# Optimization experiments

Hardware: AMD Instinct MI355X
Metric: run time of the kernel (lower is better)

## Reference

```python
import jax, jax.numpy as jnp
import numpy as np

NUM_NODES = 1_000_000
HIDDEN = 256
NUM_GRAPHS = 1024


def setup_inputs() -> dict:
    key = jax.random.key(0)
    k_x, k_b, k_w1, k_b1, k_w2, k_b2 = jax.random.split(key, 6)
    x = jax.random.normal(k_x, (NUM_NODES, HIDDEN), dtype=jnp.float32)
    batch = jnp.sort(jax.random.randint(k_b, (NUM_NODES,), 0, NUM_GRAPHS, dtype=jnp.int64))
    h = HIDDEN // 2
    # torch Linear default init: U(-1/sqrt(fan_in), 1/sqrt(fan_in))
    s1 = 1.0 / np.sqrt(HIDDEN)
    s2 = 1.0 / np.sqrt(h)
    w1 = jax.random.uniform(k_w1, (HIDDEN, h), jnp.float32, -s1, s1)
    b1 = jax.random.uniform(k_b1, (h,), jnp.float32, -s1, s1)
    w2 = jax.random.uniform(k_w2, (h, 1), jnp.float32, -s2, s2)
    b2 = jax.random.uniform(k_b2, (1,), jnp.float32, -s2, s2)
    return {"x": x, "batch": batch, "w1": w1, "b1": b1, "w2": w2, "b2": b2}


def reference(x, batch, w1, b1, w2, b2):
    # attention MLP: Linear -> tanh -> Linear -> scalar score per node
    scores = (jnp.tanh(x @ w1 + b1) @ w2 + b2)[:, 0]  # [N]
    # segment softmax over nodes of each graph (numerically stable)
    seg_max = jax.ops.segment_max(scores, batch, num_segments=NUM_GRAPHS)  # [B]
    e = jnp.exp(scores - seg_max[batch])  # [N]
    denom = jax.ops.segment_sum(e, batch, num_segments=NUM_GRAPHS)  # [B]
    attn = e / denom[batch]  # [N]
    # attention-weighted scatter-add pooling -> [B, H]
    return jax.ops.segment_sum(x * attn[:, None], batch, num_segments=NUM_GRAPHS)
```

## Files before the change

kernel.cpp:

```cpp
#include <hip/hip_runtime.h>
#include <stdint.h>

#define N_NODES 1000000
#define HID 256
#define HH  128
#define NG  1024
#define TILE 32
#define CHUNK 1984
#define NBLOCKS ((N_NODES + CHUNK - 1) / CHUNK)

typedef short short8v __attribute__((ext_vector_type(8)));
typedef float f32x4 __attribute__((ext_vector_type(4)));

#define GLOBAL_AS __attribute__((address_space(1)))
#define LDS_AS    __attribute__((address_space(3)))

__device__ __forceinline__ unsigned short f2bf(float f){
  unsigned u = __float_as_uint(f);
  u += 0x7FFFu + ((u >> 16) & 1u);
  return (unsigned short)(u >> 16);
}

__device__ __forceinline__ float fast_tanh(float v){
  float e = __expf(2.f * v);
  return 1.f - 2.f / (e + 1.f);
}

__global__ void k_prep(const float* __restrict__ w1, unsigned short* __restrict__ w1f){
  int s = blockIdx.x * blockDim.x + threadIdx.x;
  if (s >= 4096) return;
  int nt = s >> 9, rem = s & 511, ks = rem >> 6, lane = rem & 63;
  int q = lane >> 4, c = lane & 15;
  union { unsigned short u[8]; uint4 v; } tmp;
  for (int i = 0; i < 8; ++i){
    int k = ks * 32 + q * 8 + i;
    int n = nt * 16 + c;
    tmp.u[i] = f2bf(w1[k * HH + n]);
  }
  *(uint4*)(w1f + (size_t)s * 8) = tmp.v;
}

__device__ __forceinline__ void stage_tile(const float* __restrict__ x, long node0,
                                           float* lds_tile, int wave, int lane){
  #pragma unroll
  for (int rr = 0; rr < 8; ++rr){
    int r = wave * 8 + rr;
    const float* gp = x + (size_t)(node0 + r) * HID + ((lane ^ (r & 15)) << 2);
    __builtin_amdgcn_global_load_lds(
        (const GLOBAL_AS unsigned int*)gp,
        (LDS_AS unsigned int*)(lds_tile + r * HID),
        16, 0, 0);
  }
}

__global__ __launch_bounds__(256, 2) void k_fused(
    const float* __restrict__ x, const unsigned short* __restrict__ w1f,
    const float* __restrict__ b1, const float* __restrict__ w2,
    const float* __restrict__ b2, const int* __restrict__ batch,
    float* __restrict__ denom, float* __restrict__ out)
{
  __shared__ __align__(16) float xs[2][TILE * HID];
  __shared__ int   b_all[CHUNK];
  __shared__ float partial_s[4][TILE];
  __shared__ float e_s[TILE];

  const int tid = threadIdx.x;
  const long base = (long)blockIdx.x * CHUNK;
  if (base >= N_NODES) return;
  long rem = (long)N_NODES - base;
  const int nvalid = (rem < CHUNK) ? (int)rem : CHUNK;
  const int ntiles = nvalid / TILE;

  const int wave = tid >> 6, lane = tid & 63;
  const int q = lane >> 4, col = lane & 15;

  for (int i = tid; i < nvalid; i += 256) b_all[i] = batch[base + i];

  short8v wf0[8], wf1[8];
  #pragma unroll
  for (int ks = 0; ks < 8; ++ks){
    int nt0 = wave * 2;
    wf0[ks] = *(const short8v*)(w1f + (((size_t)nt0 * 8 + ks) * 64 + lane) * 8);
    wf1[ks] = *(const short8v*)(w1f + ((((size_t)nt0 + 1) * 8 + ks) * 64 + lane) * 8);
  }
  float b1v0 = b1[wave * 32 + col],      w2v0 = w2[wave * 32 + col];
  float b1v1 = b1[wave * 32 + 16 + col], w2v1 = w2[wave * 32 + 16 + col];
  const float b2v = b2[0];

  stage_tile(x, base, &xs[0][0], wave, lane);

  float accp = 0.f;
  int curg = batch[base];

  for (int t = 0; t < ntiles; ++t){
    const int par = t & 1;
    __syncthreads();

    if (t + 1 < ntiles)
      stage_tile(x, base + (long)(t + 1) * TILE, &xs[par ^ 1][0], wave, lane);

    const float* xb = &xs[par][0];

    f32x4 acc00 = {0.f,0.f,0.f,0.f}, acc01 = {0.f,0.f,0.f,0.f};
    f32x4 acc10 = {0.f,0.f,0.f,0.f}, acc11 = {0.f,0.f,0.f,0.f};
    #pragma unroll
    for (int ks = 0; ks < 8; ++ks){
      const int k16 = ks * 8 + q * 2;
      #pragma unroll
      for (int rg = 0; rg < 2; ++rg){
        const int R  = rg * 16 + col;
        const int sw = R & 15;
        f32x4 xa = *(const f32x4*)(xb + R * HID + ((k16 ^ sw) << 2));
        f32x4 xc = *(const f32x4*)(xb + R * HID + (((k16 + 1) ^ sw) << 2));
        short8v a;
        a[0] = (short)f2bf(xa[0]); a[1] = (short)f2bf(xa[1]);
        a[2] = (short)f2bf(xa[2]); a[3] = (short)f2bf(xa[3]);
        a[4] = (short)f2bf(xc[0]); a[5] = (short)f2bf(xc[1]);
        a[6] = (short)f2bf(xc[2]); a[7] = (short)f2bf(xc[3]);
        if (rg == 0){
          acc00 = __builtin_amdgcn_mfma_f32_16x16x32_bf16(a, wf0[ks], acc00, 0, 0, 0);
          acc01 = __builtin_amdgcn_mfma_f32_16x16x32_bf16(a, wf1[ks], acc01, 0, 0, 0);
        } else {
          acc10 = __builtin_amdgcn_mfma_f32_16x16x32_bf16(a, wf0[ks], acc10, 0, 0, 0);
          acc11 = __builtin_amdgcn_mfma_f32_16x16x32_bf16(a, wf1[ks], acc11, 0, 0, 0);
        }
      }
    }
    #pragma unroll
    for (int rg = 0; rg < 2; ++rg){
      #pragma unroll
      for (int r = 0; r < 4; ++r){
        float a0 = (rg == 0) ? acc00[r] : acc10[r];
        float a1 = (rg == 0) ? acc01[r] : acc11[r];
        float p = fast_tanh(a0 + b1v0) * w2v0 + fast_tanh(a1 + b1v1) * w2v1;
        p += __shfl_xor(p, 1); p += __shfl_xor(p, 2);
        p += __shfl_xor(p, 4); p += __shfl_xor(p, 8);
        if (col == r) partial_s[wave][rg * 16 + q * 4 + r] = p;
      }
    }
    __syncthreads();

    if (tid < TILE){
      float pt = partial_s[0][tid] + partial_s[1][tid]
               + partial_s[2][tid] + partial_s[3][tid];
      float e = __expf(pt + b2v);
      e_s[tid] = e;
      int b  = b_all[t * TILE + tid];
      int b0 = b_all[t * TILE];
      int bl = b_all[t * TILE + TILE - 1];
      if (b0 == bl){
        float s = e;
        s += __shfl_xor(s, 1);  s += __shfl_xor(s, 2);
        s += __shfl_xor(s, 4);  s += __shfl_xor(s, 8);
        s += __shfl_xor(s, 16);
        if (tid == 0) atomicAdd(&denom[b0], s);
      } else {
        atomicAdd(&denom[b], e);
      }
    }
    __syncthreads();

    {
      const int chi = tid >> 2, clo = tid & 3;
      #pragma unroll 8
      for (int i = 0; i < TILE; ++i){
        int b   = b_all[t * TILE + i];
        float e = e_s[i];
        float xv = xb[i * HID + ((chi ^ (i & 15)) << 2) + clo];
        if (b != curg){
          atomicAdd(&out[(size_t)curg * HID + tid], accp);
          accp = 0.f;
          curg = b;
        }
        accp += e * xv;
      }
    }
  }
  atomicAdd(&out[(size_t)curg * HID + tid], accp);
}

__global__ void k_norm(float* __restrict__ out, const float* __restrict__ denom){
  int g = blockIdx.x, c = threadIdx.x;
  float d = denom[g];
  size_t idx = (size_t)g * HID + c;
  float o = out[idx];
  out[idx] = (d > 0.f) ? __fdividef(o, d) : 0.f;
}

extern "C" void kernel_launch(void* const* d_in, const int* in_sizes, int n_in,
                              void* d_out, int out_size, void* d_ws, size_t ws_size,
                              hipStream_t stream){
  const float* x     = (const float*)d_in[0];
  const int*   batch = (const int*)d_in[1];
  const float* w1    = (const float*)d_in[2];
  const float* b1    = (const float*)d_in[3];
  const float* w2    = (const float*)d_in[4];
  const float* b2    = (const float*)d_in[5];
  float* out = (float*)d_out;

  char* ws = (char*)d_ws;
  unsigned short* w1f = (unsigned short*)ws;
  float* denom = (float*)(ws + 65536);

  hipMemsetAsync(denom, 0, 4096, stream);
  hipMemsetAsync(d_out, 0, (size_t)out_size * sizeof(float), stream);

  k_prep<<<16, 256, 0, stream>>>(w1, w1f);
  k_fused<<<NBLOCKS, 256, 0, stream>>>(x, w1f, b1, w2, b2, batch, denom, out);
  k_norm<<<NG, 256, 0, stream>>>(out, denom);
}
```

Baseline: 1.485 ms.

## Compute softmax weights redundantly per wave, drop barrier, split tile prefetch

Each wave now computes the exponentiated scores itself from partial_s and broadcasts them with a lane shuffle. This removes the e_s shared buffer and one __syncthreads per tile. The next-tile prefetch is split into two halves, with the second half issued after the score phase, to spread out the async global-to-LDS loads. The pooling loop is also fully unrolled. The cost is redundant exp work in every wave and a later start for half of the prefetch.

```diff
diff --git a/kernel.cpp b/kernel.cpp
--- a/kernel.cpp
+++ b/kernel.cpp
@@ -40,10 +40,10 @@
   *(uint4*)(w1f + (size_t)s * 8) = tmp.v;
 }
 
-__device__ __forceinline__ void stage_tile(const float* __restrict__ x, long node0,
-                                           float* lds_tile, int wave, int lane){
+__device__ __forceinline__ void stage_half(const float* __restrict__ x, long node0,
+                                           float* lds_tile, int wave, int lane, int half){
   #pragma unroll
-  for (int rr = 0; rr < 8; ++rr){
+  for (int rr = half * 4; rr < half * 4 + 4; ++rr){
     int r = wave * 8 + rr;
     const float* gp = x + (size_t)(node0 + r) * HID + ((lane ^ (r & 15)) << 2);
     __builtin_amdgcn_global_load_lds(
@@ -62,7 +62,6 @@
   __shared__ __align__(16) float xs[2][TILE * HID];
   __shared__ int   b_all[CHUNK];
   __shared__ float partial_s[4][TILE];
-  __shared__ float e_s[TILE];
 
   const int tid = threadIdx.x;
   const long base = (long)blockIdx.x * CHUNK;
@@ -87,7 +86,8 @@
   float b1v1 = b1[wave * 32 + 16 + col], w2v1 = w2[wave * 32 + 16 + col];
   const float b2v = b2[0];
 
-  stage_tile(x, base, &xs[0][0], wave, lane);
+  stage_half(x, base, &xs[0][0], wave, lane, 0);
+  stage_half(x, base, &xs[0][0], wave, lane, 1);
 
   float accp = 0.f;
   int curg = batch[base];
@@ -97,7 +97,7 @@
     __syncthreads();
 
     if (t + 1 < ntiles)
-      stage_tile(x, base + (long)(t + 1) * TILE, &xs[par ^ 1][0], wave, lane);
+      stage_half(x, base + (long)(t + 1) * TILE, &xs[par ^ 1][0], wave, lane, 0);
 
     const float* xb = &xs[par][0];
 
@@ -140,32 +140,37 @@
     }
     __syncthreads();
 
-    if (tid < TILE){
-      float pt = partial_s[0][tid] + partial_s[1][tid]
-               + partial_s[2][tid] + partial_s[3][tid];
-      float e = __expf(pt + b2v);
-      e_s[tid] = e;
-      int b  = b_all[t * TILE + tid];
-      int b0 = b_all[t * TILE];
-      int bl = b_all[t * TILE + TILE - 1];
+    float e_reg;
+    {
+      const int l32 = lane & 31;
+      float pt = partial_s[0][l32] + partial_s[1][l32]
+               + partial_s[2][l32] + partial_s[3][l32];
+      e_reg = __expf(pt + b2v);
+    }
+    if (wave == 0){
+      const int i0 = t * TILE;
+      int b0 = b_all[i0];
+      int bl = b_all[i0 + TILE - 1];
       if (b0 == bl){
-        float s = e;
+        float s = e_reg;
         s += __shfl_xor(s, 1);  s += __shfl_xor(s, 2);
         s += __shfl_xor(s, 4);  s += __shfl_xor(s, 8);
         s += __shfl_xor(s, 16);
-        if (tid == 0) atomicAdd(&denom[b0], s);
-      } else {
-        atomicAdd(&denom[b], e);
-      }
-    }
-    __syncthreads();
+        if (lane == 0) atomicAdd(&denom[b0], s);
+      } else if (lane < TILE){
+        atomicAdd(&denom[b_all[i0 + lane]], e_reg);
+      }
+    }
+
+    if (t + 1 < ntiles)
+      stage_half(x, base + (long)(t + 1) * TILE, &xs[par ^ 1][0], wave, lane, 1);
 
     {
       const int chi = tid >> 2, clo = tid & 3;
-      #pragma unroll 8
+      #pragma unroll
       for (int i = 0; i < TILE; ++i){
         int b   = b_all[t * TILE + i];
-        float e = e_s[i];
+        float e = __shfl(e_reg, i);
         float xv = xb[i * HID + ((chi ^ (i & 15)) << 2) + clo];
         if (b != curg){
           atomicAdd(&out[(size_t)curg * HID + tid], accp);
```

Result: no change. 1.475 ms (-0.7%).
